# Performance work log

Measured on AMD Instinct MI355X. Metric: run time of the kernel, lower is better.

The kernel has to match this reference:

```python
import jax, jax.numpy as jnp
import numpy as np

E = 8      # num_experts
D = 1024   # input_size
H = 1024   # head_size
K = 2      # top-k


def setup_inputs() -> dict:
    key = jax.random.key(0)
    k1, k2, k3, k4, k5, k6 = jax.random.split(key, 6)
    x = jax.random.normal(k1, (4, 1024, D), dtype=jnp.float32)
    # ParallelExperts init: uniform(-1/fan_in, 1/fan_in)
    w1 = jax.random.uniform(k2, (E, D, H), jnp.float32, -1.0 / D, 1.0 / D)
    b1 = jax.random.uniform(k3, (E, H), jnp.float32, -1.0 / np.sqrt(D), 1.0 / np.sqrt(D))
    w2 = jax.random.uniform(k4, (E, H, D), jnp.float32, -1.0 / H, 1.0 / H)
    b2 = jax.random.uniform(k5, (E, D), jnp.float32, -1.0 / np.sqrt(H), 1.0 / np.sqrt(H))
    # gate Linear(input_size, num_experts, bias=False); scaled so softmax isn't saturated
    wg = jax.random.normal(k6, (D, E), dtype=jnp.float32) * 0.02
    return {"x": x, "w1": w1, "b1": b1, "w2": w2, "b2": b2, "wg": wg}


def reference(x, w1, b1, w2, b2, wg):
    bsz, length, d = x.shape
    xf = x.reshape(-1, d)                                  # [T, D]
    # --- top_k_gating (noisy_gating=False, no skip_mask) ---
    logits = xf @ wg                                       # [T, E]
    probs = jax.nn.softmax(logits, axis=-1)
    top_v, top_i = jax.lax.top_k(probs, K)                 # [T, K]
    top_v = top_v / (jnp.sum(top_v, axis=-1, keepdims=True) + 1e-6)
    # dense combine weights: gate[t, e] = renormalized prob if e in top-k else 0
    gates = jnp.sum(jax.nn.one_hot(top_i, E, dtype=xf.dtype) * top_v[..., None], axis=1)  # [T, E]
    # --- map: per-expert first GEMM + bias (dense formulation == grouped GEMM, no drops) ---
    h = jnp.einsum('td,edh->teh', xf, w1) + b1[None]       # [T, E, H]
    # --- activation between map and reduce (nn.GELU, exact erf form) ---
    a = jax.nn.gelu(h, approximate=False)
    # --- reduce: per-expert second GEMM + bias, scaled by gate, scatter-add back ---
    o = jnp.einsum('teh,ehd->ted', a, w2) + b2[None]       # [T, E, D]
    y = jnp.einsum('te,ted->td', gates, o)                 # [T, D]
    return y.reshape(bsz, length, d)
```

## Files before the change

### kernel.cpp

```cpp
#include <hip/hip_runtime.h>
#include <hip/hip_bf16.h>
#include <math.h>

#define TT 4096
#define EE 8
#define DD 1024
#define HH 1024
#define CAP 4096

typedef __attribute__((ext_vector_type(8))) short bf16x8;
typedef __attribute__((ext_vector_type(4))) float f32x4;

#define GLL16(gp, lp)                                                                   \
    __builtin_amdgcn_global_load_lds((__attribute__((address_space(1))) void*)(gp),     \
                                     (__attribute__((address_space(3))) void*)(lp),     \
                                     16, 0, 0)

static const size_t OFF_XB     = 0;
static const size_t OFF_W1T    = 8u * 1024 * 1024;
static const size_t OFF_W2T    = 24u * 1024 * 1024;
static const size_t OFF_ABUF   = 40u * 1024 * 1024;
static const size_t OFF_OBUF   = 56u * 1024 * 1024;
static const size_t OFF_ROWMAP = 88u * 1024 * 1024;
static const size_t OFF_GATES  = OFF_ROWMAP + 8 * CAP * 4;
static const size_t OFF_COUNTS = OFF_GATES + 8192 * 4;
static const size_t OFF_PICKS  = OFF_COUNTS + 256;

__global__ __launch_bounds__(256) void gate_compute(
    const float* __restrict__ x, const float* __restrict__ wg,
    __hip_bfloat16* __restrict__ xb, int* __restrict__ picks,
    float* __restrict__ gates)
{
    const int lane = threadIdx.x & 63;
    const int wave = threadIdx.x >> 6;
    const int tbase = blockIdx.x * 16 + wave * 4;

    for (int i = 0; i < 4; ++i) {
        const int t = tbase + i;
        const float4* xr = (const float4*)(x + (size_t)t * DD);
        ushort4* xbr = (ushort4*)(xb + (size_t)t * DD);

        float acc[EE];
#pragma unroll
        for (int e = 0; e < EE; ++e) acc[e] = 0.f;

#pragma unroll
        for (int c = 0; c < 4; ++c) {
            const int v4 = lane + 64 * c;
            float4 xv = xr[v4];
            __hip_bfloat16 h0 = __float2bfloat16(xv.x);
            __hip_bfloat16 h1 = __float2bfloat16(xv.y);
            __hip_bfloat16 h2 = __float2bfloat16(xv.z);
            __hip_bfloat16 h3 = __float2bfloat16(xv.w);
            ushort4 s;
            s.x = *(unsigned short*)&h0; s.y = *(unsigned short*)&h1;
            s.z = *(unsigned short*)&h2; s.w = *(unsigned short*)&h3;
            xbr[v4] = s;
            const float4* wrow = (const float4*)(wg + (size_t)(4 * v4) * EE);
            const float xs[4] = {xv.x, xv.y, xv.z, xv.w};
#pragma unroll
            for (int q = 0; q < 4; ++q) {
                float4 w0 = wrow[q * 2];
                float4 w1v = wrow[q * 2 + 1];
                acc[0] = fmaf(xs[q], w0.x, acc[0]);
                acc[1] = fmaf(xs[q], w0.y, acc[1]);
                acc[2] = fmaf(xs[q], w0.z, acc[2]);
                acc[3] = fmaf(xs[q], w0.w, acc[3]);
                acc[4] = fmaf(xs[q], w1v.x, acc[4]);
                acc[5] = fmaf(xs[q], w1v.y, acc[5]);
                acc[6] = fmaf(xs[q], w1v.z, acc[6]);
                acc[7] = fmaf(xs[q], w1v.w, acc[7]);
            }
        }
#pragma unroll
        for (int off = 32; off > 0; off >>= 1) {
#pragma unroll
            for (int e = 0; e < EE; ++e) acc[e] += __shfl_xor(acc[e], off, 64);
        }
        if (lane == 0) {
            float mx = acc[0];
#pragma unroll
            for (int e = 1; e < EE; ++e) mx = fmaxf(mx, acc[e]);
            float p[EE];
            float s = 0.f;
#pragma unroll
            for (int e = 0; e < EE; ++e) { p[e] = expf(acc[e] - mx); s += p[e]; }
            int i0 = 0;
#pragma unroll
            for (int e = 1; e < EE; ++e) if (acc[e] > acc[i0]) i0 = e;
            int i1 = (i0 == 0) ? 1 : 0;
#pragma unroll
            for (int e = 0; e < EE; ++e) {
                if (e != i0 && acc[e] > acc[i1]) i1 = e;
            }
            float v0 = p[i0] / s, v1 = p[i1] / s;
            float den = v0 + v1 + 1e-6f;
            gates[t * 2 + 0] = v0 / den;
            gates[t * 2 + 1] = v1 / den;
            picks[t] = i0 | (i1 << 4);
        }
    }
}

__global__ __launch_bounds__(256) void bucket_build(
    const int* __restrict__ picks, int* __restrict__ rowmap, int* __restrict__ counts)
{
    const int e = blockIdx.x;
    const int tid = threadIdx.x;
    const int lane = tid & 63;
    const int wave = tid >> 6;
    __shared__ int wsum[4];

    int runtot = 0;
    for (int tb = 0; tb < TT; tb += 256) {
        const int t = tb + tid;
        const int p = picks[t];
        const int m0 = ((p & 15) == e) ? 1 : 0;
        const int m1 = (((p >> 4) & 15) == e) ? 1 : 0;
        const int c = m0 + m1;
        int incl = c;
#pragma unroll
        for (int off = 1; off < 64; off <<= 1) {
            int v = __shfl_up(incl, off, 64);
            if (lane >= off) incl += v;
        }
        if (lane == 63) wsum[wave] = incl;
        __syncthreads();
        int wbase = 0;
#pragma unroll
        for (int w = 0; w < 4; ++w) wbase += (w < wave) ? wsum[w] : 0;
        int slot = runtot + wbase + incl - c;
        if (m0) { rowmap[e * CAP + slot] = t * 2; slot += 1; }
        if (m1) { rowmap[e * CAP + slot] = t * 2 + 1; }
        runtot += wsum[0] + wsum[1] + wsum[2] + wsum[3];
        __syncthreads();
    }
    if (tid == 0) counts[e] = runtot;
}

__global__ __launch_bounds__(256) void transpose_cvt(
    const float* __restrict__ w1, const float* __restrict__ w2,
    __hip_bfloat16* __restrict__ w1t, __hip_bfloat16* __restrict__ w2t)
{
    __shared__ float tile[32][33];
    const int z = blockIdx.z;
    const float* src = (z < EE ? w1 : w2) + (size_t)(z & 7) * DD * HH;
    __hip_bfloat16* dst = (z < EE ? w1t : w2t) + (size_t)(z & 7) * DD * HH;
    const int bx = blockIdx.x * 32, by = blockIdx.y * 32;
    const int tx = threadIdx.x & 31, ty = threadIdx.x >> 5;
#pragma unroll
    for (int i = 0; i < 4; ++i)
        tile[ty + 8 * i][tx] = src[(size_t)(by + ty + 8 * i) * 1024 + bx + tx];
    __syncthreads();
#pragma unroll
    for (int i = 0; i < 4; ++i)
        dst[(size_t)(bx + ty + 8 * i) * 1024 + by + tx] = __float2bfloat16(tile[tx][ty + 8 * i]);
}

template <int LAYER>
__global__ __launch_bounds__(256) void moe_gemm(
    const __hip_bfloat16* __restrict__ Abase,
    const __hip_bfloat16* __restrict__ Bbase,
    const float* __restrict__ bias,
    const int* __restrict__ rowmap,
    const int* __restrict__ counts,
    const float* __restrict__ gates,
    void* __restrict__ OutP)
{
    const int e = blockIdx.z;
    const int cnt = counts[e];
    const int m0 = blockIdx.y * 128;
    if (m0 >= cnt) return;
    const int n0 = blockIdx.x * 128;
    const int tid = threadIdx.x;
    const int lane = tid & 63;
    const int wave = tid >> 6;
    const int wm = (wave >> 1) * 64;
    const int wn = (wave & 1) * 64;
    const int lrow = lane & 15;
    const int quad = lane >> 4;

    __shared__ __hip_bfloat16 As[128 * 32];
    __shared__ __hip_bfloat16 Bs[128 * 32];

    const int ar0 = m0 + (tid >> 2);
    const int ar1 = ar0 + 64;
    const int e0 = rowmap[e * CAP + (ar0 < cnt ? ar0 : 0)];
    const int e1 = rowmap[e * CAP + (ar1 < cnt ? ar1 : 0)];
    const size_t src0 = (size_t)(LAYER == 1 ? (e0 >> 1) : e0);
    const size_t src1 = (size_t)(LAYER == 1 ? (e1 >> 1) : e1);
    const __hip_bfloat16* gA0 = Abase + src0 * DD + (tid & 3) * 8;
    const __hip_bfloat16* gA1 = Abase + src1 * DD + (tid & 3) * 8;
    const __hip_bfloat16* Bexp = Bbase + (size_t)e * DD * HH;
    const __hip_bfloat16* gB0 = Bexp + (size_t)(n0 + (tid >> 2)) * DD + (tid & 3) * 8;
    const __hip_bfloat16* gB1 = gB0 + (size_t)64 * DD;

    char* ldsA0 = (char*)As + wave * 1024;
    char* ldsA1 = (char*)As + 4096 + wave * 1024;
    char* ldsB0 = (char*)Bs + wave * 1024;
    char* ldsB1 = (char*)Bs + 4096 + wave * 1024;

    f32x4 acc[4][4];
#pragma unroll
    for (int i = 0; i < 4; ++i)
#pragma unroll
        for (int j = 0; j < 4; ++j) acc[i][j] = (f32x4){0.f, 0.f, 0.f, 0.f};

    const bf16x8* Av = (const bf16x8*)As;
    const bf16x8* Bv = (const bf16x8*)Bs;

    for (int kt = 0; kt < DD / 32; ++kt) {
        const int ko = kt * 32;
        GLL16(gA0 + ko, ldsA0);
        GLL16(gA1 + ko, ldsA1);
        GLL16(gB0 + ko, ldsB0);
        GLL16(gB1 + ko, ldsB1);
        __syncthreads();

        bf16x8 af[4], bfr[4];
#pragma unroll
        for (int i = 0; i < 4; ++i) {
            af[i]  = Av[(wm + i * 16 + lrow) * 4 + quad];
            bfr[i] = Bv[(wn + i * 16 + lrow) * 4 + quad];
        }
#pragma unroll
        for (int mi = 0; mi < 4; ++mi)
#pragma unroll
            for (int ni = 0; ni < 4; ++ni)
                acc[mi][ni] = __builtin_amdgcn_mfma_f32_16x16x32_bf16(
                    af[mi], bfr[ni], acc[mi][ni], 0, 0, 0);
        __syncthreads();
    }

    if (LAYER == 1) {
        __hip_bfloat16* abuf = (__hip_bfloat16*)OutP;
#pragma unroll
        for (int mi = 0; mi < 4; ++mi) {
#pragma unroll
            for (int r = 0; r < 4; ++r) {
                const int mrow = wm + mi * 16 + quad * 4 + r;
                const int gm = m0 + mrow;
                if (gm < cnt) {
                    const int ent = rowmap[e * CAP + gm];
                    __hip_bfloat16* orow = abuf + (size_t)ent * HH + n0 + wn + lrow;
#pragma unroll
                    for (int ni = 0; ni < 4; ++ni) {
                        float v = acc[mi][ni][r] + bias[e * HH + n0 + wn + ni * 16 + lrow];
                        v = 0.5f * v * (1.f + erff(v * 0.70710678118654752f));
                        orow[ni * 16] = __float2bfloat16(v);
                    }
                }
            }
        }
    } else {
        float* obuf = (float*)OutP;
#pragma unroll
        for (int mi = 0; mi < 4; ++mi) {
#pragma unroll
            for (int r = 0; r < 4; ++r) {
                const int mrow = wm + mi * 16 + quad * 4 + r;
                const int gm = m0 + mrow;
                if (gm < cnt) {
                    const int ent = rowmap[e * CAP + gm];
                    const float g = gates[ent];
                    float* orow = obuf + (size_t)ent * DD + n0 + wn + lrow;
#pragma unroll
                    for (int ni = 0; ni < 4; ++ni) {
                        float v = acc[mi][ni][r] + bias[e * DD + n0 + wn + ni * 16 + lrow];
                        orow[ni * 16] = v * g;
                    }
                }
            }
        }
    }
}

__global__ __launch_bounds__(256) void combine_kernel(
    const float* __restrict__ obuf, float* __restrict__ y)
{
    const size_t i = (size_t)blockIdx.x * 256 + threadIdx.x;
    const size_t t = i >> 8;
    const size_t c = i & 255;
    const float4* o0 = (const float4*)(obuf + t * 2 * DD);
    float4 a = o0[c];
    float4 b = o0[256 + c];
    float4 r;
    r.x = a.x + b.x; r.y = a.y + b.y; r.z = a.z + b.z; r.w = a.w + b.w;
    ((float4*)y)[i] = r;
}

extern "C" void kernel_launch(void* const* d_in, const int* in_sizes, int n_in,
                              void* d_out, int out_size, void* d_ws, size_t ws_size,
                              hipStream_t stream)
{
    const float* x  = (const float*)d_in[0];
    const float* w1 = (const float*)d_in[1];
    const float* b1 = (const float*)d_in[2];
    const float* w2 = (const float*)d_in[3];
    const float* b2 = (const float*)d_in[4];
    const float* wg = (const float*)d_in[5];
    float* y = (float*)d_out;

    char* ws = (char*)d_ws;
    __hip_bfloat16* xb   = (__hip_bfloat16*)(ws + OFF_XB);
    __hip_bfloat16* w1t  = (__hip_bfloat16*)(ws + OFF_W1T);
    __hip_bfloat16* w2t  = (__hip_bfloat16*)(ws + OFF_W2T);
    __hip_bfloat16* abuf = (__hip_bfloat16*)(ws + OFF_ABUF);
    float* obuf  = (float*)(ws + OFF_OBUF);
    int*   rowmap = (int*)(ws + OFF_ROWMAP);
    float* gates  = (float*)(ws + OFF_GATES);
    int*   counts = (int*)(ws + OFF_COUNTS);
    int*   picks  = (int*)(ws + OFF_PICKS);

    gate_compute<<<TT / 16, 256, 0, stream>>>(x, wg, xb, picks, gates);
    bucket_build<<<EE, 256, 0, stream>>>(picks, rowmap, counts);
    transpose_cvt<<<dim3(32, 32, 16), 256, 0, stream>>>(w1, w2, w1t, w2t);
    moe_gemm<1><<<dim3(HH / 128, CAP / 128, EE), 256, 0, stream>>>(
        xb, w1t, b1, rowmap, counts, gates, (void*)abuf);
    moe_gemm<2><<<dim3(DD / 128, CAP / 128, EE), 256, 0, stream>>>(
        abuf, w2t, b2, rowmap, counts, gates, (void*)obuf);
    combine_kernel<<<TT * DD / 4 / 256, 256, 0, stream>>>(obuf, y);
}
```

Before: 241.2 us.

## Fuse weight transpose into gate kernel and deepen GEMM K-step to 128

Merges the weight transpose/bf16 conversion into the gating kernel as extra blocks, using 64x64 tiles with float4 loads and vectorized stores, which drops one launch and widens memory accesses. The MoE GEMM now loads four 32-wide K slices into LDS per barrier pair instead of one, cutting barriers per K by four. This raises LDS use to 64KB per block, which can lower occupancy.

```diff
diff --git a/kernel.cpp b/kernel.cpp
--- a/kernel.cpp
+++ b/kernel.cpp
@@ -26,14 +26,57 @@
 static const size_t OFF_COUNTS = OFF_GATES + 8192 * 4;
 static const size_t OFF_PICKS  = OFF_COUNTS + 256;
 
-__global__ __launch_bounds__(256) void gate_compute(
+__global__ __launch_bounds__(256) void prep_kernel(
     const float* __restrict__ x, const float* __restrict__ wg,
-    __hip_bfloat16* __restrict__ xb, int* __restrict__ picks,
-    float* __restrict__ gates)
-{
-    const int lane = threadIdx.x & 63;
-    const int wave = threadIdx.x >> 6;
-    const int tbase = blockIdx.x * 16 + wave * 4;
+    const float* __restrict__ w1, const float* __restrict__ w2,
+    __hip_bfloat16* __restrict__ xb,
+    __hip_bfloat16* __restrict__ w1t, __hip_bfloat16* __restrict__ w2t,
+    int* __restrict__ picks, float* __restrict__ gates)
+{
+    __shared__ float tl[64][65];
+    const int bid = blockIdx.x;
+    const int tid = threadIdx.x;
+
+    if (bid < 4096) {
+        const int mat = bid >> 8;
+        const int tt = bid & 255;
+        const int R = (tt >> 4) * 64;
+        const int C = (tt & 15) * 64;
+        const float* src = (mat < EE ? w1 : w2) + (size_t)(mat & 7) * DD * HH;
+        __hip_bfloat16* dst = (mat < EE ? w1t : w2t) + (size_t)(mat & 7) * DD * HH;
+
+        const int lrow = tid >> 4;
+        const int c4 = tid & 15;
+#pragma unroll
+        for (int i = 0; i < 4; ++i) {
+            const int r = lrow + i * 16;
+            float4 v = *(const float4*)(src + (size_t)(R + r) * 1024 + C + c4 * 4);
+            tl[r][c4 * 4 + 0] = v.x;
+            tl[r][c4 * 4 + 1] = v.y;
+            tl[r][c4 * 4 + 2] = v.z;
+            tl[r][c4 * 4 + 3] = v.w;
+        }
+        __syncthreads();
+        const int seg = tid & 7;
+        const int orow0 = tid >> 3;
+#pragma unroll
+        for (int p = 0; p < 2; ++p) {
+            const int orow = orow0 + p * 32;
+            unsigned short u[8];
+#pragma unroll
+            for (int j = 0; j < 8; ++j) {
+                __hip_bfloat16 h = __float2bfloat16(tl[seg * 8 + j][orow]);
+                u[j] = *(unsigned short*)&h;
+            }
+            *(ushort4*)(dst + (size_t)(C + orow) * 1024 + R + seg * 8)     = (ushort4){u[0], u[1], u[2], u[3]};
+            *(ushort4*)(dst + (size_t)(C + orow) * 1024 + R + seg * 8 + 4) = (ushort4){u[4], u[5], u[6], u[7]};
+        }
+        return;
+    }
+
+    const int lane = tid & 63;
+    const int wave = tid >> 6;
+    const int tbase = (bid - 4096) * 16 + wave * 4;
 
     for (int i = 0; i < 4; ++i) {
         const int t = tbase + i;
@@ -138,25 +181,6 @@
     if (tid == 0) counts[e] = runtot;
 }
 
-__global__ __launch_bounds__(256) void transpose_cvt(
-    const float* __restrict__ w1, const float* __restrict__ w2,
-    __hip_bfloat16* __restrict__ w1t, __hip_bfloat16* __restrict__ w2t)
-{
-    __shared__ float tile[32][33];
-    const int z = blockIdx.z;
-    const float* src = (z < EE ? w1 : w2) + (size_t)(z & 7) * DD * HH;
-    __hip_bfloat16* dst = (z < EE ? w1t : w2t) + (size_t)(z & 7) * DD * HH;
-    const int bx = blockIdx.x * 32, by = blockIdx.y * 32;
-    const int tx = threadIdx.x & 31, ty = threadIdx.x >> 5;
-#pragma unroll
-    for (int i = 0; i < 4; ++i)
-        tile[ty + 8 * i][tx] = src[(size_t)(by + ty + 8 * i) * 1024 + bx + tx];
-    __syncthreads();
-#pragma unroll
-    for (int i = 0; i < 4; ++i)
-        dst[(size_t)(bx + ty + 8 * i) * 1024 + by + tx] = __float2bfloat16(tile[tx][ty + 8 * i]);
-}
-
 template <int LAYER>
 __global__ __launch_bounds__(256) void moe_gemm(
     const __hip_bfloat16* __restrict__ Abase,
@@ -180,8 +204,8 @@
     const int lrow = lane & 15;
     const int quad = lane >> 4;
 
-    __shared__ __hip_bfloat16 As[128 * 32];
-    __shared__ __hip_bfloat16 Bs[128 * 32];
+    __shared__ __hip_bfloat16 As[4][128 * 32];
+    __shared__ __hip_bfloat16 Bs[4][128 * 32];
 
     const int ar0 = m0 + (tid >> 2);
     const int ar1 = ar0 + 64;
@@ -195,40 +219,42 @@
     const __hip_bfloat16* gB0 = Bexp + (size_t)(n0 + (tid >> 2)) * DD + (tid & 3) * 8;
     const __hip_bfloat16* gB1 = gB0 + (size_t)64 * DD;
 
-    char* ldsA0 = (char*)As + wave * 1024;
-    char* ldsA1 = (char*)As + 4096 + wave * 1024;
-    char* ldsB0 = (char*)Bs + wave * 1024;
-    char* ldsB1 = (char*)Bs + 4096 + wave * 1024;
-
     f32x4 acc[4][4];
 #pragma unroll
     for (int i = 0; i < 4; ++i)
 #pragma unroll
         for (int j = 0; j < 4; ++j) acc[i][j] = (f32x4){0.f, 0.f, 0.f, 0.f};
 
-    const bf16x8* Av = (const bf16x8*)As;
-    const bf16x8* Bv = (const bf16x8*)Bs;
-
-    for (int kt = 0; kt < DD / 32; ++kt) {
-        const int ko = kt * 32;
-        GLL16(gA0 + ko, ldsA0);
-        GLL16(gA1 + ko, ldsA1);
-        GLL16(gB0 + ko, ldsB0);
-        GLL16(gB1 + ko, ldsB1);
-        __syncthreads();
-
-        bf16x8 af[4], bfr[4];
-#pragma unroll
-        for (int i = 0; i < 4; ++i) {
-            af[i]  = Av[(wm + i * 16 + lrow) * 4 + quad];
-            bfr[i] = Bv[(wn + i * 16 + lrow) * 4 + quad];
-        }
-#pragma unroll
-        for (int mi = 0; mi < 4; ++mi)
-#pragma unroll
-            for (int ni = 0; ni < 4; ++ni)
-                acc[mi][ni] = __builtin_amdgcn_mfma_f32_16x16x32_bf16(
-                    af[mi], bfr[ni], acc[mi][ni], 0, 0, 0);
+    for (int kt = 0; kt < DD / 128; ++kt) {
+#pragma unroll
+        for (int s = 0; s < 4; ++s) {
+            const int ko = kt * 128 + s * 32;
+            char* lA = (char*)&As[s][0] + wave * 1024;
+            char* lB = (char*)&Bs[s][0] + wave * 1024;
+            GLL16(gA0 + ko, lA);
+            GLL16(gA1 + ko, lA + 4096);
+            GLL16(gB0 + ko, lB);
+            GLL16(gB1 + ko, lB + 4096);
+        }
+        __syncthreads();
+
+#pragma unroll
+        for (int s = 0; s < 4; ++s) {
+            const bf16x8* Av = (const bf16x8*)&As[s][0];
+            const bf16x8* Bv = (const bf16x8*)&Bs[s][0];
+            bf16x8 af[4], bfr[4];
+#pragma unroll
+            for (int i = 0; i < 4; ++i) {
+                af[i]  = Av[(wm + i * 16 + lrow) * 4 + quad];
+                bfr[i] = Bv[(wn + i * 16 + lrow) * 4 + quad];
+            }
+#pragma unroll
+            for (int mi = 0; mi < 4; ++mi)
+#pragma unroll
+                for (int ni = 0; ni < 4; ++ni)
+                    acc[mi][ni] = __builtin_amdgcn_mfma_f32_16x16x32_bf16(
+                        af[mi], bfr[ni], acc[mi][ni], 0, 0, 0);
+        }
         __syncthreads();
     }
 
@@ -312,9 +338,8 @@
     int*   counts = (int*)(ws + OFF_COUNTS);
     int*   picks  = (int*)(ws + OFF_PICKS);
 
-    gate_compute<<<TT / 16, 256, 0, stream>>>(x, wg, xb, picks, gates);
+    prep_kernel<<<4096 + 256, 256, 0, stream>>>(x, wg, w1, w2, xb, w1t, w2t, picks, gates);
     bucket_build<<<EE, 256, 0, stream>>>(picks, rowmap, counts);
-    transpose_cvt<<<dim3(32, 32, 16), 256, 0, stream>>>(w1, w2, w1t, w2t);
     moe_gemm<1><<<dim3(HH / 128, CAP / 128, EE), 256, 0, stream>>>(
         xb, w1t, b1, rowmap, counts, gates, (void*)abuf);
     moe_gemm<2><<<dim3(DD / 128, CAP / 128, EE), 256, 0, stream>>>(
```

Result: slower. 257.0 us (+6.5%).
